# Performance work log

Hardware: AMD Instinct MI355X
Metric: run time of the kernel (lower is better)

## Reference

```python
import jax, jax.numpy as jnp
import numpy as np

N = 100_000      # nodes
E = 3_200_000    # edges
F_IN = 9
F_HID = 9
F_OUT = 1
EPS = 1e-5

def _ln(x, g, b):
    m = x.mean(-1, keepdims=True)
    v = x.var(-1, keepdims=True)
    return (x - m) / jnp.sqrt(v + EPS) * g + b

def _gat(x, src, dst, edge_attr, W, a_src, a_dst, We, a_e, bias):
    # Single-head GATConv with edge_dim=1, add_self_loops=True, fill_value='mean'
    n = x.shape[0]
    loop = jnp.arange(n)
    deg = jax.ops.segment_sum(jnp.ones((src.shape[0],), x.dtype), dst, n)
    loop_attr = jax.ops.segment_sum(edge_attr, dst, n) / jnp.maximum(deg, 1.0)[:, None]
    s = jnp.concatenate([src, loop])
    d = jnp.concatenate([dst, loop])
    ea = jnp.concatenate([edge_attr, loop_attr], axis=0)   # [E+N, 1]
    xp = x @ W                                             # [N, C]
    a = (xp * a_src).sum(-1)[s] + (xp * a_dst).sum(-1)[d] + ((ea @ We) * a_e).sum(-1)
    a = jax.nn.leaky_relu(a, 0.2)
    amax = jax.ops.segment_max(a, d, n)
    aexp = jnp.exp(a - amax[d])
    denom = jax.ops.segment_sum(aexp, d, n)
    alpha = aexp / (denom[d] + 1e-16)
    return jax.ops.segment_sum(alpha[:, None] * xp[s], d, n) + bias

def setup_inputs() -> dict:
    key = jax.random.key(0)
    ks = jax.random.split(key, 16)
    def rn(k, shp, s):
        return jax.random.normal(k, shp, jnp.float32) * s
    return {
        "x": jax.random.normal(ks[0], (N, F_IN), jnp.float32),
        "edge_index": jax.random.randint(ks[1], (2, E), 0, N, jnp.int32),
        "edge_attr": jax.random.normal(ks[2], (E, 1), jnp.float32),
        "ln1_g": jnp.ones((F_IN,), jnp.float32), "ln1_b": jnp.zeros((F_IN,), jnp.float32),
        "W0": rn(ks[3], (F_IN, F_HID), 0.3), "as0": rn(ks[4], (F_HID,), 0.3),
        "ad0": rn(ks[5], (F_HID,), 0.3), "We0": rn(ks[6], (1, F_HID), 0.3),
        "ae0": rn(ks[7], (F_HID,), 0.3), "b0": jnp.zeros((F_HID,), jnp.float32),
        "W1": rn(ks[8], (F_HID, F_HID), 0.3), "as1": rn(ks[9], (F_HID,), 0.3),
        "ad1": rn(ks[10], (F_HID,), 0.3), "We1": rn(ks[11], (1, F_HID), 0.3),
        "ae1": rn(ks[12], (F_HID,), 0.3), "b1": jnp.zeros((F_HID,), jnp.float32),
        "ng1": jnp.ones((F_HID,), jnp.float32), "nb1": jnp.zeros((F_HID,), jnp.float32),
        "ln2_g": jnp.ones((2 * F_HID,), jnp.float32), "ln2_b": jnp.zeros((2 * F_HID,), jnp.float32),
        "et_W": rn(ks[13], (2 * F_HID, F_HID), 0.2), "et_b": jnp.zeros((F_HID,), jnp.float32),
        "fc_W": rn(ks[14], (F_HID, F_OUT), 0.3), "fc_b": jnp.zeros((F_OUT,), jnp.float32),
        "att_W": rn(ks[15], (2 * F_OUT, F_OUT), 0.5), "att_b": jnp.zeros((F_OUT,), jnp.float32),
    }

def reference(x, edge_index, edge_attr, ln1_g, ln1_b, W0, as0, ad0, We0, ae0, b0,
              W1, as1, ad1, We1, ae1, b1, ng1, nb1, ln2_g, ln2_b,
              et_W, et_b, fc_W, fc_b, att_W, att_b):
    src, dst = edge_index[0], edge_index[1]
    h = _ln(x, ln1_g, ln1_b)
    # layer 0: no norm/residual
    h = jax.nn.leaky_relu(_gat(h, src, dst, edge_attr, W0, as0, ad0, We0, ae0, b0), 0.01)
    # layer 1: norm + residual
    ident = h
    h = _ln(_gat(h, src, dst, edge_attr, W1, as1, ad1, We1, ae1, b1), ng1, nb1) + ident
    h = jax.nn.leaky_relu(h, 0.01)
    # edge path: gather-concat-norm-MLP  [E, 2H]
    ef = _ln(jnp.concatenate([h[src], h[dst]], axis=1), ln2_g, ln2_b)
    eo = jax.nn.leaky_relu(ef @ et_W + et_b, 0.01)
    eo = eo @ fc_W + fc_b                       # [E, 1]
    # AttentionLayer
    comb = jnp.concatenate([eo, edge_attr], axis=1)   # [E, 2]
    w = jax.nn.softmax(comb @ att_W + att_b, axis=-1) # [E, 1]
    att = (w * comb).sum(axis=1, keepdims=True)       # [E, 1]
    return att + eo
```

## Files before the change

kernel.cpp:

```cpp
#include <hip/hip_runtime.h>
#include <hip/hip_bf16.h>
#include <hip/hip_fp16.h>

typedef __hip_bfloat16 bf16;
typedef unsigned int uint;
typedef unsigned short ushort;
#define TPB 256
#define TPBS 512
#define TPBG 512
#define BSH 7
#define BNODES 128
#define NBK_MAX 1024
#define CH 8192
#define EPT (CH / TPBS)
#define CAP 4608

enum {
  LN1G = 0, LN1B = 9, PW0 = 18, AS0 = 99, AD0 = 108, CE0 = 117, B0 = 118,
  PW1 = 127, AS1 = 208, AD1 = 217, CE1 = 226, B1 = 227, NG = 236, NB = 245,
  LN2G = 254, LN2B = 272, ETW = 290, ETB = 452, FCW = 461, FCB = 470,
  GC = 471, KC = 480, NPARAM = 489
};

static __device__ __forceinline__ float lrelu(float x, float s) { return x >= 0.f ? x : s * x; }
static __device__ __forceinline__ float ldx(const void* p, long i, int isb) {
    return isb ? __bfloat162float(((const bf16*)p)[i]) : ((const float*)p)[i];
}
static __device__ __forceinline__ uint bfb(float f) {
    uint u = __float_as_uint(f);
    return (u + 0x7FFFu + ((u >> 16) & 1u)) >> 16;
}
static __device__ __forceinline__ uint pack2(float a, float b) { return bfb(a) | (bfb(b) << 16); }
static __device__ __forceinline__ float unlo(uint u) { return __uint_as_float(u << 16); }
static __device__ __forceinline__ float unhi(uint u) { return __uint_as_float(u & 0xFFFF0000u); }
static __device__ __forceinline__ ushort h16(float f) { return __half_as_ushort(__float2half(f)); }
static __device__ __forceinline__ uint p2h(float a, float b) { return (uint)h16(a) | ((uint)h16(b) << 16); }
static __device__ __forceinline__ float hfl(uint u) { return __half2float(__ushort_as_half((ushort)(u & 0xFFFFu))); }
static __device__ __forceinline__ float hfh(uint u) { return __half2float(__ushort_as_half((ushort)(u >> 16))); }
static __device__ __forceinline__ float hfs(ushort u) { return __half2float(__ushort_as_half(u)); }

__global__ void k_params(const void* ln1g, const void* ln1b,
                         const void* W0, const void* as0, const void* ad0,
                         const void* We0, const void* ae0, const void* b0,
                         const void* W1, const void* as1, const void* ad1,
                         const void* We1, const void* ae1, const void* b1,
                         const void* ng, const void* nb,
                         const void* ln2g, const void* ln2b,
                         const void* etW, const void* etb,
                         const void* fcW, const void* fcb,
                         float* __restrict__ P, int* __restrict__ flagp,
                         int* __restrict__ gcursor, int nbk)
{
    __shared__ int sflag;
    if (threadIdx.x == 0) {
        unsigned short h0 = ((const unsigned short*)ln1g)[0];
        sflag = (h0 == 0x3F80u) ? 1 : 0;
        *flagp = sflag;
    }
    __syncthreads();
    const int f = sflag;
    const int t = threadIdx.x;
    for (int j = t; j < nbk; j += TPB) gcursor[j] = j * CAP;
    for (int i = t; i < 9; i += TPB) {
        P[LN1G + i] = ldx(ln1g, i, f); P[LN1B + i] = ldx(ln1b, i, f);
        P[AS0 + i] = ldx(as0, i, f);   P[AD0 + i] = ldx(ad0, i, f);
        P[B0 + i]  = ldx(b0, i, f);
        P[AS1 + i] = ldx(as1, i, f);   P[AD1 + i] = ldx(ad1, i, f);
        P[B1 + i]  = ldx(b1, i, f);
        P[NG + i]  = ldx(ng, i, f);    P[NB + i]  = ldx(nb, i, f);
        P[ETB + i] = ldx(etb, i, f);   P[FCW + i] = ldx(fcW, i, f);
    }
    for (int i = t; i < 81; i += TPB) { P[PW0 + i] = ldx(W0, i, f); P[PW1 + i] = ldx(W1, i, f); }
    for (int i = t; i < 18; i += TPB) { P[LN2G + i] = ldx(ln2g, i, f); P[LN2B + i] = ldx(ln2b, i, f); }
    for (int i = t; i < 162; i += TPB) P[ETW + i] = ldx(etW, i, f) * ldx(ln2g, i / 9, f);
    if (t == 0) {
        float c0 = 0.f, c1 = 0.f;
        for (int k = 0; k < 9; k++) {
            c0 += ldx(We0, k, f) * ldx(ae0, k, f);
            c1 += ldx(We1, k, f) * ldx(ae1, k, f);
        }
        P[CE0] = c0; P[CE1] = c1; P[FCB] = ldx(fcb, 0, f);
        for (int c = 0; c < 9; c++) {
            float gc = 0.f, kc = 0.f;
            for (int k = 0; k < 18; k++) {
                float wv = ldx(etW, (long)k * 9 + c, f);
                gc += ldx(ln2g, k, f) * wv;
                kc += ldx(ln2b, k, f) * wv;
            }
            P[GC + c] = gc * (1.f / 18.f);
            P[KC + c] = kc + ldx(etb, c, f);
        }
    }
}

__global__ void __launch_bounds__(TPBS)
k_bscatter(const int* __restrict__ src, const int* __restrict__ dst,
           const void* __restrict__ ea, const int* __restrict__ flagp,
           int* __restrict__ gcursor, int2* __restrict__ ebuf, int e, int nbk)
{
    __shared__ int cnt[NBK_MAX];
    __shared__ int cur[NBK_MAX];
    const int tid = threadIdx.x;
    const int s0 = blockIdx.x * CH;
    const int m = min(e - s0, CH);
    for (int j = tid; j < nbk; j += TPBS) cnt[j] = 0;
    __syncthreads();
    int dreg[EPT];
    #pragma unroll
    for (int k = 0; k < EPT; k++) {
        int t = tid + k * TPBS;
        dreg[k] = (t < m) ? dst[s0 + t] : -1;
        if (t < m) atomicAdd(&cnt[dreg[k] >> BSH], 1);
    }
    __syncthreads();
    for (int j = tid; j < nbk; j += TPBS) {
        int c = cnt[j];
        cur[j] = c ? atomicAdd(&gcursor[j], c) : 0;
    }
    __syncthreads();
    const int fl = *flagp;
    #pragma unroll
    for (int k = 0; k < EPT; k++) {
        int t = tid + k * TPBS;
        if (t < m) {
            int d = dreg[k];
            int b = d >> BSH;
            int pos = atomicAdd(&cur[b], 1);
            if (pos < (b + 1) * CAP) {
                float eav = ldx(ea, s0 + t, fl);
                ebuf[pos] = make_int2(src[s0 + t] | ((d & (BNODES - 1)) << 17),
                                      __float_as_int(eav));
            }
        }
    }
}

__global__ void k_prep(const void* __restrict__ x, const float* __restrict__ P,
                       const int* __restrict__ flagp,
                       uint* __restrict__ xpb0, float* __restrict__ sd0, int n)
{
    const int fl = *flagp;
    int i = blockIdx.x * blockDim.x + threadIdx.x;
    if (i >= n) return;
    float h[9]; float m = 0.f;
    #pragma unroll
    for (int f = 0; f < 9; f++) { h[f] = ldx(x, (long)i * 9 + f, fl); m += h[f]; }
    m *= (1.f / 9.f);
    float v = 0.f;
    #pragma unroll
    for (int f = 0; f < 9; f++) { float d = h[f] - m; v += d * d; }
    float r = rsqrtf(v * (1.f / 9.f) + 1e-5f);
    #pragma unroll
    for (int f = 0; f < 9; f++) h[f] = (h[f] - m) * r * P[LN1G + f] + P[LN1B + f];
    float xr[9]; float ss = 0.f, sd = 0.f;
    #pragma unroll
    for (int c = 0; c < 9; c++) {
        float acc = 0.f;
        #pragma unroll
        for (int f = 0; f < 9; f++) acc += h[f] * P[PW0 + f * 9 + c];
        xr[c] = acc;
        ss += acc * P[AS0 + c]; sd += acc * P[AD0 + c];
    }
    uint* row = xpb0 + (size_t)i * 8;
    ((uint4*)row)[0] = make_uint4(pack2(xr[0], xr[1]), pack2(xr[2], xr[3]),
                                  pack2(xr[4], xr[5]), pack2(xr[6], xr[7]));
    ((uint4*)row)[1] = make_uint4(pack2(xr[8], ss), 0u, 0u, 0u);
    sd0[i] = sd;
}

__global__ void __launch_bounds__(TPBG)
k_sortg0(const int* __restrict__ gcursor, const int2* __restrict__ ebuf,
         const float* __restrict__ P,
         const uint* __restrict__ xpb0, const float* __restrict__ sd0,
         float* __restrict__ h1, uint* __restrict__ xpb1,
         float* __restrict__ sd1, float* __restrict__ la, int n)
{
    __shared__ int2 seb[CAP];
    __shared__ ushort sidx[CAP];
    __shared__ int hist[BNODES], scn[BNODES], cur[BNODES];
    const int b = blockIdx.x, tid = threadIdx.x;
    const int beg = b * CAP;
    int cnt = gcursor[b] - beg;
    if (cnt > CAP) cnt = CAP;
    if (cnt < 0) cnt = 0;
    for (int j = tid; j < BNODES; j += TPBG) hist[j] = 0;
    __syncthreads();
    for (int j = tid; j < cnt; j += TPBG) {
        int2 v = ebuf[beg + j];
        seb[j] = v;
        atomicAdd(&hist[(v.x >> 17) & (BNODES - 1)], 1);
    }
    __syncthreads();
    if (tid < BNODES) scn[tid] = hist[tid];
    __syncthreads();
    for (int off = 1; off < BNODES; off <<= 1) {
        int v2 = 0;
        if (tid < BNODES) v2 = scn[tid] + (tid >= off ? scn[tid - off] : 0);
        __syncthreads();
        if (tid < BNODES) scn[tid] = v2;
        __syncthreads();
    }
    if (tid < BNODES) cur[tid] = scn[tid] - hist[tid];
    __syncthreads();
    for (int j = tid; j < cnt; j += TPBG) {
        int dl = (seb[j].x >> 17) & (BNODES - 1);
        int slot = atomicAdd(&cur[dl], 1);
        sidx[slot] = (ushort)j;
    }
    __syncthreads();
    const int nd = tid >> 2, l = tid & 3;
    const int i = (b << BSH) + nd;
    if (i < n) {
        const float ce = P[CE0];
        const int locend = scn[nd], locbeg = locend - hist[nd];
        const float sdi = sd0[i];
        float acc[11];
        #pragma unroll
        for (int k = 0; k < 11; k++) acc[k] = 0.f;
        for (int j = locbeg + l; j < locend; j += 4) {
            int2 sl = seb[sidx[j]];
            int s = sl.x & 0x1FFFF;
            float eav = __int_as_float(sl.y);
            const uint* row = xpb0 + (size_t)s * 8;
            uint4 q0 = *(const uint4*)row;
            uint  q2 = row[4];
            float ex = expf(lrelu(unhi(q2) + sdi + ce * eav, 0.2f));
            acc[0] += ex; acc[1] += eav;
            acc[2] += ex * unlo(q0.x); acc[3] += ex * unhi(q0.x);
            acc[4] += ex * unlo(q0.y); acc[5] += ex * unhi(q0.y);
            acc[6] += ex * unlo(q0.z); acc[7] += ex * unhi(q0.z);
            acc[8] += ex * unlo(q0.w); acc[9] += ex * unhi(q0.w);
            acc[10] += ex * unlo(q2);
        }
        #pragma unroll
        for (int k = 0; k < 11; k++) {
            acc[k] += __shfl_xor(acc[k], 1, 64);
            acc[k] += __shfl_xor(acc[k], 2, 64);
        }
        if (l == 0) {
            float denom = acc[0];
            float S[9] = {acc[2], acc[3], acc[4], acc[5], acc[6], acc[7], acc[8], acc[9], acc[10]};
            float deg = (float)hist[nd];
            float lav = acc[1] / fmaxf(deg, 1.f);
            la[i] = lav;
            const uint* row = xpb0 + (size_t)i * 8;
            uint4 q0 = *(const uint4*)row;
            uint  q2 = row[4];
            float o0 = unlo(q0.x), o1 = unhi(q0.x), o2 = unlo(q0.y), o3 = unhi(q0.y);
            float o4 = unlo(q0.z), o5 = unhi(q0.z), o6 = unlo(q0.w), o7 = unhi(q0.w);
            float o8 = unlo(q2),   ssi = unhi(q2);
            float ex0 = expf(lrelu(ssi + sdi + ce * lav, 0.2f));
            denom += ex0;
            S[0] += ex0 * o0; S[1] += ex0 * o1; S[2] += ex0 * o2; S[3] += ex0 * o3;
            S[4] += ex0 * o4; S[5] += ex0 * o5; S[6] += ex0 * o6; S[7] += ex0 * o7;
            S[8] += ex0 * o8;
            float inv = 1.f / (denom + 1e-16f);
            float h[9];
            #pragma unroll
            for (int c = 0; c < 9; c++) h[c] = lrelu(S[c] * inv + P[B0 + c], 0.01f);
            float4* hr = (float4*)(h1 + (size_t)i * 12);
            hr[0] = make_float4(h[0], h[1], h[2], h[3]);
            hr[1] = make_float4(h[4], h[5], h[6], h[7]);
            hr[2] = make_float4(h[8], 0.f, 0.f, 0.f);
            float xr1[9]; float ss2 = 0.f, sd2 = 0.f;
            #pragma unroll
            for (int c = 0; c < 9; c++) {
                float a2 = 0.f;
                #pragma unroll
                for (int f = 0; f < 9; f++) a2 += h[f] * P[PW1 + f * 9 + c];
                xr1[c] = a2;
                ss2 += a2 * P[AS1 + c]; sd2 += a2 * P[AD1 + c];
            }
            uint* rw = xpb1 + (size_t)i * 8;
            ((uint4*)rw)[0] = make_uint4(pack2(xr1[0], xr1[1]), pack2(xr1[2], xr1[3]),
                                         pack2(xr1[4], xr1[5]), pack2(xr1[6], xr1[7]));
            ((uint4*)rw)[1] = make_uint4(pack2(xr1[8], ss2), 0u, 0u, 0u);
            sd1[i] = sd2;
        }
    }
}

__global__ void __launch_bounds__(TPBG)
k_sortg1(const int* __restrict__ gcursor, const int2* __restrict__ ebuf,
         const float* __restrict__ P,
         const uint* __restrict__ xpb1, const float* __restrict__ sd1,
         const float* __restrict__ la, const float* __restrict__ h1,
         uint4* __restrict__ uarr, uint4* __restrict__ warr, int n)
{
    __shared__ int2 seb[CAP];
    __shared__ ushort sidx[CAP];
    __shared__ int hist[BNODES], scn[BNODES], cur[BNODES];
    const int b = blockIdx.x, tid = threadIdx.x;
    const int beg = b * CAP;
    int cnt = gcursor[b] - beg;
    if (cnt > CAP) cnt = CAP;
    if (cnt < 0) cnt = 0;
    for (int j = tid; j < BNODES; j += TPBG) hist[j] = 0;
    __syncthreads();
    for (int j = tid; j < cnt; j += TPBG) {
        int2 v = ebuf[beg + j];
        seb[j] = v;
        atomicAdd(&hist[(v.x >> 17) & (BNODES - 1)], 1);
    }
    __syncthreads();
    if (tid < BNODES) scn[tid] = hist[tid];
    __syncthreads();
    for (int off = 1; off < BNODES; off <<= 1) {
        int v2 = 0;
        if (tid < BNODES) v2 = scn[tid] + (tid >= off ? scn[tid - off] : 0);
        __syncthreads();
        if (tid < BNODES) scn[tid] = v2;
        __syncthreads();
    }
    if (tid < BNODES) cur[tid] = scn[tid] - hist[tid];
    __syncthreads();
    for (int j = tid; j < cnt; j += TPBG) {
        int dl = (seb[j].x >> 17) & (BNODES - 1);
        int slot = atomicAdd(&cur[dl], 1);
        sidx[slot] = (ushort)j;
    }
    __syncthreads();
    const int nd = tid >> 2, l = tid & 3;
    const int i = (b << BSH) + nd;
    if (i < n) {
        const float ce = P[CE1];
        const int locend = scn[nd], locbeg = locend - hist[nd];
        const float sdi = sd1[i];
        float acc[10];
        #pragma unroll
        for (int k = 0; k < 10; k++) acc[k] = 0.f;
        for (int j = locbeg + l; j < locend; j += 4) {
            int2 sl = seb[sidx[j]];
            int s = sl.x & 0x1FFFF;
            float eav = __int_as_float(sl.y);
            const uint* row = xpb1 + (size_t)s * 8;
            uint4 q0 = *(const uint4*)row;
            uint  q2 = row[4];
            float ex = expf(lrelu(unhi(q2) + sdi + ce * eav, 0.2f));
            acc[0] += ex;
            acc[1] += ex * unlo(q0.x); acc[2] += ex * unhi(q0.x);
            acc[3] += ex * unlo(q0.y); acc[4] += ex * unhi(q0.y);
            acc[5] += ex * unlo(q0.z); acc[6] += ex * unhi(q0.z);
            acc[7] += ex * unlo(q0.w); acc[8] += ex * unhi(q0.w);
            acc[9] += ex * unlo(q2);
        }
        #pragma unroll
        for (int k = 0; k < 10; k++) {
            acc[k] += __shfl_xor(acc[k], 1, 64);
            acc[k] += __shfl_xor(acc[k], 2, 64);
        }
        if (l == 0) {
            float denom = acc[0];
            float S[9] = {acc[1], acc[2], acc[3], acc[4], acc[5], acc[6], acc[7], acc[8], acc[9]};
            const uint* row = xpb1 + (size_t)i * 8;
            uint4 q0 = *(const uint4*)row;
            uint  q2 = row[4];
            float o0 = unlo(q0.x), o1 = unhi(q0.x), o2 = unlo(q0.y), o3 = unhi(q0.y);
            float o4 = unlo(q0.z), o5 = unhi(q0.z), o6 = unlo(q0.w), o7 = unhi(q0.w);
            float o8 = unlo(q2),   ssi = unhi(q2);
            float ex0 = expf(lrelu(ssi + sdi + ce * la[i], 0.2f));
            denom += ex0;
            S[0] += ex0 * o0; S[1] += ex0 * o1; S[2] += ex0 * o2; S[3] += ex0 * o3;
            S[4] += ex0 * o4; S[5] += ex0 * o5; S[6] += ex0 * o6; S[7] += ex0 * o7;
            S[8] += ex0 * o8;
            float inv = 1.f / (denom + 1e-16f);
            float g[9]; float m = 0.f;
            #pragma unroll
            for (int c = 0; c < 9; c++) { g[c] = S[c] * inv + P[B1 + c]; m += g[c]; }
            m *= (1.f / 9.f);
            float v = 0.f;
            #pragma unroll
            for (int c = 0; c < 9; c++) { float d = g[c] - m; v += d * d; }
            float r = rsqrtf(v * (1.f / 9.f) + 1e-5f);
            const float4* hr = (const float4*)(h1 + (size_t)i * 12);
            float4 r0 = hr[0], r1 = hr[1], r2 = hr[2];
            float res[9] = {r0.x, r0.y, r0.z, r0.w, r1.x, r1.y, r1.z, r1.w, r2.x};
            float o[9];
            #pragma unroll
            for (int c = 0; c < 9; c++)
                o[c] = lrelu((g[c] - m) * r * P[NG + c] + P[NB + c] + res[c], 0.01f);
            float psum = 0.f, pss = 0.f;
            #pragma unroll
            for (int c = 0; c < 9; c++) { psum += o[c]; pss += o[c] * o[c]; }
            uint sumb = __float_as_uint(psum * (1.f / 18.f));
            uint ssb  = __float_as_uint(pss * (1.f / 18.f));
            float u[9];
            #pragma unroll
            for (int c = 0; c < 9; c++) {
                float a2 = 0.f;
                #pragma unroll
                for (int k = 0; k < 9; k++) a2 += o[k] * P[ETW + k * 9 + c];
                u[c] = a2 - psum * P[GC + c];
            }
            uint4* up = uarr + (size_t)i * 2;
            up[0] = make_uint4(p2h(u[0], u[1]), p2h(u[2], u[3]), p2h(u[4], u[5]), p2h(u[6], u[7]));
            up[1] = make_uint4((uint)h16(u[8]), sumb, ssb, 0u);
            #pragma unroll
            for (int c = 0; c < 9; c++) {
                float a2 = 0.f;
                #pragma unroll
                for (int k = 0; k < 9; k++) a2 += o[k] * P[ETW + (9 + k) * 9 + c];
                u[c] = a2 - psum * P[GC + c];
            }
            uint4* wp = warr + (size_t)i * 2;
            wp[0] = make_uint4(p2h(u[0], u[1]), p2h(u[2], u[3]), p2h(u[4], u[5]), p2h(u[6], u[7]));
            wp[1] = make_uint4((uint)h16(u[8]), sumb, ssb, 0u);
        }
    }
}

__global__ void __launch_bounds__(TPB)
k_edge(const int* __restrict__ src, const int* __restrict__ dst,
       const void* __restrict__ ea, const float* __restrict__ P,
       const int* __restrict__ flagp,
       const uint4* __restrict__ uarr, const uint4* __restrict__ warr,
       void* __restrict__ outp, int e)
{
    const int fl = *flagp;
    int t = blockIdx.x * blockDim.x + threadIdx.x;
    if (t >= e) return;
    int s = src[t], d = dst[t];
    const uint4* up = uarr + (size_t)s * 2;
    const uint4* wp = warr + (size_t)d * 2;
    uint4 a0 = up[0], a1 = up[1];
    uint4 b0 = wp[0], b1 = wp[1];
    float m   = __uint_as_float(a1.y) + __uint_as_float(b1.y);
    float ex2 = __uint_as_float(a1.z) + __uint_as_float(b1.z);
    float r = rsqrtf(fmaxf(ex2 - m * m, 0.f) + 1e-5f);
    float uv[9] = {hfl(a0.x) + hfl(b0.x), hfh(a0.x) + hfh(b0.x),
                   hfl(a0.y) + hfl(b0.y), hfh(a0.y) + hfh(b0.y),
                   hfl(a0.z) + hfl(b0.z), hfh(a0.z) + hfh(b0.z),
                   hfl(a0.w) + hfl(b0.w), hfh(a0.w) + hfh(b0.w),
                   hfs((ushort)(a1.x & 0xFFFFu)) + hfs((ushort)(b1.x & 0xFFFFu))};
    float eo = P[FCB];
    #pragma unroll
    for (int c = 0; c < 9; c++) {
        float pre = fmaf(r, uv[c], P[KC + c]);
        float act = fmaxf(pre, 0.01f * pre);
        eo = fmaf(act, P[FCW + c], eo);
    }
    float resv = 2.f * eo + ldx(ea, t, fl);
    if (fl) ((bf16*)outp)[t] = __float2bfloat16(resv);
    else    ((float*)outp)[t] = resv;
}

extern "C" void kernel_launch(void* const* d_in, const int* in_sizes, int n_in,
                              void* d_out, int out_size, void* d_ws, size_t ws_size,
                              hipStream_t stream) {
    const int n = in_sizes[0] / 9;
    const int e = in_sizes[2];
    const int nbk = (n + BNODES - 1) >> BSH;

    const void* X   = d_in[0];
    const int*  ei  = (const int*)d_in[1];
    const int*  src = ei;
    const int*  dst = ei + e;
    const void* EA  = d_in[2];

    char* base = (char*)d_ws;
    size_t off = 0;
    auto alloc = [&](size_t bytes) { void* p = base + off; off += (bytes + 63) & ~size_t(63); return p; };
    float*  P       = (float*)alloc(512 * sizeof(float));
    int*    flagp   = (int*)(P + NPARAM);
    int*    gcursor = (int*)alloc((size_t)NBK_MAX * sizeof(int));
    int2*   ebuf    = (int2*)alloc((size_t)nbk * CAP * sizeof(int2));
    uint*   xpb0    = (uint*)alloc((size_t)n * 8 * sizeof(uint));
    uint*   xpb1    = (uint*)alloc((size_t)n * 8 * sizeof(uint));
    float*  h1      = (float*)alloc((size_t)n * 12 * sizeof(float));
    uint4*  uarr    = (uint4*)alloc((size_t)n * 2 * sizeof(uint4));
    uint4*  warr    = (uint4*)alloc((size_t)n * 2 * sizeof(uint4));
    float*  sd0     = (float*)alloc((size_t)n * sizeof(float));
    float*  sd1     = (float*)alloc((size_t)n * sizeof(float));
    float*  la      = (float*)alloc((size_t)n * sizeof(float));

    dim3 gN((n + TPB - 1) / TPB);
    dim3 gE((e + TPB - 1) / TPB);
    dim3 gC((e + CH - 1) / CH);
    dim3 gB(nbk);

    k_params<<<1, TPB, 0, stream>>>(d_in[3], d_in[4], d_in[5], d_in[6], d_in[7],
                                    d_in[8], d_in[9], d_in[10], d_in[11], d_in[12],
                                    d_in[13], d_in[14], d_in[15], d_in[16], d_in[17],
                                    d_in[18], d_in[19], d_in[20], d_in[21], d_in[22],
                                    d_in[23], d_in[24], P, flagp, gcursor, nbk);
    k_prep<<<gN, dim3(TPB), 0, stream>>>(X, P, flagp, xpb0, sd0, n);
    k_bscatter<<<gC, dim3(TPBS), 0, stream>>>(src, dst, EA, flagp, gcursor, ebuf, e, nbk);
    k_sortg0<<<gB, dim3(TPBG), 0, stream>>>(gcursor, ebuf, P, xpb0, sd0, h1, xpb1, sd1, la, n);
    k_sortg1<<<gB, dim3(TPBG), 0, stream>>>(gcursor, ebuf, P, xpb1, sd1, la, h1, uarr, warr, n);
    k_edge<<<gE, dim3(TPB), 0, stream>>>(src, dst, EA, P, flagp, uarr, warr, d_out, e);
}
```

Baseline: 206.8 us.

## Locally sort edges by bucket in shared memory before scattering to global buffer

The bucket scatter kernel now does a block-wide exclusive scan of per-bucket counts, places edge indices into a shared-memory staging array grouped by bucket, and then writes to the global edge buffer in bucket-contiguous order. This makes the global writes to ebuf more coalesced than the previous random per-edge scattered writes. The chunk size is halved to fit the shared staging array, which doubles the number of blocks and global cursor atomics. It also assumes nbk <= 1024, since counts are now initialized and scanned for exactly 2*TPBS buckets.

```diff
diff --git a/kernel.cpp b/kernel.cpp
--- a/kernel.cpp
+++ b/kernel.cpp
@@ -11,8 +11,9 @@
 #define BSH 7
 #define BNODES 128
 #define NBK_MAX 1024
-#define CH 8192
+#define CH 4096
 #define EPT (CH / TPBS)
+#define NW (TPBS / 64)
 #define CAP 4608
 
 enum {
@@ -99,11 +100,17 @@
            int* __restrict__ gcursor, int2* __restrict__ ebuf, int e, int nbk)
 {
     __shared__ int cnt[NBK_MAX];
+    __shared__ int exs[NBK_MAX];
+    __shared__ int base[NBK_MAX];
     __shared__ int cur[NBK_MAX];
+    __shared__ int wsum[NW];
+    __shared__ uint sidx[CH];
     const int tid = threadIdx.x;
+    const int lane = tid & 63;
+    const int wid = tid >> 6;
     const int s0 = blockIdx.x * CH;
     const int m = min(e - s0, CH);
-    for (int j = tid; j < nbk; j += TPBS) cnt[j] = 0;
+    cnt[tid] = 0; cnt[tid + TPBS] = 0;
     __syncthreads();
     int dreg[EPT];
     #pragma unroll
@@ -113,23 +120,51 @@
         if (t < m) atomicAdd(&cnt[dreg[k] >> BSH], 1);
     }
     __syncthreads();
-    for (int j = tid; j < nbk; j += TPBS) {
-        int c = cnt[j];
-        cur[j] = c ? atomicAdd(&gcursor[j], c) : 0;
-    }
-    __syncthreads();
-    const int fl = *flagp;
+    const int j0 = tid * 2, j1 = j0 + 1;
+    int c0 = cnt[j0], c1 = cnt[j1];
+    int lsum = c0 + c1;
+    int sc = lsum;
+    #pragma unroll
+    for (int o = 1; o < 64; o <<= 1) {
+        int v = __shfl_up(sc, o, 64);
+        if (lane >= o) sc += v;
+    }
+    if (lane == 63) wsum[wid] = sc;
+    __syncthreads();
+    int woff = 0;
+    #pragma unroll
+    for (int w = 0; w < NW; w++) woff += (w < wid) ? wsum[w] : 0;
+    int e0 = woff + sc - lsum;
+    int e1 = e0 + c0;
+    exs[j0] = e0; exs[j1] = e1;
+    cur[j0] = e0; cur[j1] = e1;
+    base[j0] = c0 ? atomicAdd(&gcursor[j0], c0) : 0;
+    base[j1] = c1 ? atomicAdd(&gcursor[j1], c1) : 0;
+    __syncthreads();
     #pragma unroll
     for (int k = 0; k < EPT; k++) {
         int t = tid + k * TPBS;
         if (t < m) {
             int d = dreg[k];
             int b = d >> BSH;
-            int pos = atomicAdd(&cur[b], 1);
+            int slot = atomicAdd(&cur[b], 1);
+            sidx[slot] = (uint)t | (((uint)d & (BNODES - 1)) << 13) | ((uint)b << 20);
+        }
+    }
+    __syncthreads();
+    const int fl = *flagp;
+    #pragma unroll
+    for (int k = 0; k < EPT; k++) {
+        int j = tid + k * TPBS;
+        if (j < m) {
+            uint u = sidx[j];
+            int t = u & 0x1FFF;
+            int dl = (u >> 13) & (BNODES - 1);
+            int b = u >> 20;
+            int pos = base[b] + (j - exs[b]);
             if (pos < (b + 1) * CAP) {
                 float eav = ldx(ea, s0 + t, fl);
-                ebuf[pos] = make_int2(src[s0 + t] | ((d & (BNODES - 1)) << 17),
-                                      __float_as_int(eav));
+                ebuf[pos] = make_int2(src[s0 + t] | (dl << 17), __float_as_int(eav));
             }
         }
     }
```

Result: slower. 222.6 us (+7.6%).
